# Optimization experiments

Hardware: AMD Instinct MI355X
Metric: run time of the kernel (lower is better)

The kernel has to match this reference:

```python
import jax, jax.numpy as jnp
import numpy as np

N = 16384
IN_DIM = 32
HID = 32
OUT_DIM = 16
BN_EPS = 1e-5


def setup_inputs() -> dict:
    key = jax.random.key(0)
    ks = jax.random.split(key, 8)
    x = jax.random.normal(ks[0], (N, IN_DIM), dtype=jnp.float32)
    # binary adjacency (edge existence only); avg degree ~33
    adj = jax.random.bernoulli(ks[1], 0.002, (N, N)).astype(jnp.int32)
    W1 = jax.random.normal(ks[2], (IN_DIM, HID), dtype=jnp.float32) * 0.05
    b1 = jnp.zeros((HID,), dtype=jnp.float32)
    gamma = jnp.ones((HID,), dtype=jnp.float32)
    beta = jnp.zeros((HID,), dtype=jnp.float32)
    W2 = jax.random.normal(ks[3], (HID, HID), dtype=jnp.float32) * 0.05
    b2 = jnp.zeros((HID,), dtype=jnp.float32)
    Wf = jax.random.normal(ks[4], (HID, OUT_DIM), dtype=jnp.float32) * 0.05
    bf = jnp.zeros((OUT_DIM,), dtype=jnp.float32)
    return {"x": x, "adj": adj, "W1": W1, "b1": b1, "gamma": gamma,
            "beta": beta, "W2": W2, "b2": b2, "Wf": Wf, "bf": bf}


def reference(x, adj, W1, b1, gamma, beta, W2, b2, Wf, bf):
    # GIN aggregation: for edge (src=row, dst=col) in dense_to_sparse(adj),
    # agg[dst] = sum over src of x[src]  ==  adj^T @ x  (binary adj)
    a = adj.astype(x.dtype)
    agg = jnp.einsum('ji,jd->id', a, x)  # (N, IN_DIM)
    h = x + agg  # eps = 0 default in GINConv: (1+eps)*x + agg
    # MLP: Linear -> BatchNorm1d (training stats) -> ReLU -> Linear -> ReLU
    h = h @ W1 + b1  # (N, HID)
    mu = jnp.mean(h, axis=0)
    var = jnp.mean((h - mu) ** 2, axis=0)  # biased variance (torch training mode)
    h = (h - mu) * jax.lax.rsqrt(var + BN_EPS) * gamma + beta
    h = jax.nn.relu(h)
    h = jax.nn.relu(h @ W2 + b2)  # (N, HID)
    # global mean pool over the single graph, then FC
    h_pool = jnp.mean(h, axis=0, keepdims=True)  # (1, HID)
    return h_pool @ Wf + bf  # (1, OUT_DIM)
```

## Files before the change

### kernel.cpp

```cpp
#include <hip/hip_runtime.h>

#define NN 16384
#define DD 32
#define NJ 8
#define TPB1 128
#define JCH (NN / NJ)
#define TPB2 64

template<int ATOMIC>
__global__ __launch_bounds__(TPB1) void k_agg(const int* __restrict__ adj,
                                              const float* __restrict__ x,
                                              float* __restrict__ part) {
  const int i = blockIdx.x * TPB1 + threadIdx.x;
  const int c = blockIdx.y;
  const size_t j0 = (size_t)c * JCH;
  float acc[DD];
#pragma unroll
  for (int d = 0; d < DD; ++d) acc[d] = 0.f;
  int any = 0;
  const int* p = adj + j0 * NN + i;
  for (int jj = 0; jj < JCH; jj += 8) {
    int v[8];
#pragma unroll
    for (int u = 0; u < 8; ++u) v[u] = __builtin_nontemporal_load(p + (size_t)u * NN);
    p += (size_t)8 * NN;
#pragma unroll
    for (int u = 0; u < 8; ++u) {
      if (v[u]) {
        any = 1;
        const float4* xr = (const float4*)(x + (j0 + jj + u) * DD);
#pragma unroll
        for (int q = 0; q < 8; ++q) {
          float4 xv = xr[q];
          acc[4*q+0] += xv.x; acc[4*q+1] += xv.y;
          acc[4*q+2] += xv.z; acc[4*q+3] += xv.w;
        }
      }
    }
  }
  if (ATOMIC) {
    if (any) {
      float* dst = part + (size_t)i * DD;
#pragma unroll
      for (int d = 0; d < DD; ++d) atomicAdd(dst + d, acc[d]);
    }
  } else {
    float4* dst = (float4*)(part + ((size_t)c * NN + i) * DD);
#pragma unroll
    for (int q = 0; q < 8; ++q)
      dst[q] = make_float4(acc[4*q], acc[4*q+1], acc[4*q+2], acc[4*q+3]);
  }
}

__global__ __launch_bounds__(TPB2) void k_mlp1(const float* __restrict__ x,
                                               const float* __restrict__ part, int nbuf,
                                               const float* __restrict__ W1,
                                               const float* __restrict__ b1,
                                               float* __restrict__ h1,
                                               float* __restrict__ stats) {
  __shared__ float sW[DD * DD];
  __shared__ float sb[DD];
  for (int t = threadIdx.x; t < DD * DD; t += TPB2) sW[t] = W1[t];
  if (threadIdx.x < DD) sb[threadIdx.x] = b1[threadIdx.x];
  __syncthreads();
  const int i = blockIdx.x * TPB2 + threadIdx.x;
  float hin[DD];
  const float4* xr = (const float4*)(x + (size_t)i * DD);
#pragma unroll
  for (int q = 0; q < 8; ++q) {
    float4 v = xr[q];
    hin[4*q] = v.x; hin[4*q+1] = v.y; hin[4*q+2] = v.z; hin[4*q+3] = v.w;
  }
  for (int c = 0; c < nbuf; ++c) {
    const float4* pr = (const float4*)(part + ((size_t)c * NN + i) * DD);
#pragma unroll
    for (int q = 0; q < 8; ++q) {
      float4 v = pr[q];
      hin[4*q] += v.x; hin[4*q+1] += v.y; hin[4*q+2] += v.z; hin[4*q+3] += v.w;
    }
  }
  float h[DD];
#pragma unroll
  for (int d = 0; d < DD; ++d) h[d] = sb[d];
  const float4* sW4 = (const float4*)sW;
#pragma unroll 4
  for (int k = 0; k < DD; ++k) {
    float hk = hin[k];
#pragma unroll
    for (int q = 0; q < 8; ++q) {
      float4 w = sW4[k*8 + q];
      h[4*q+0] += hk*w.x; h[4*q+1] += hk*w.y;
      h[4*q+2] += hk*w.z; h[4*q+3] += hk*w.w;
    }
  }
  float4* hw = (float4*)(h1 + (size_t)i * DD);
#pragma unroll
  for (int q = 0; q < 8; ++q)
    hw[q] = make_float4(h[4*q], h[4*q+1], h[4*q+2], h[4*q+3]);
#pragma unroll
  for (int d = 0; d < DD; ++d) {
    float s = h[d], ss = h[d] * h[d];
#pragma unroll
    for (int off = 32; off > 0; off >>= 1) {
      s += __shfl_xor(s, off);
      ss += __shfl_xor(ss, off);
    }
    if (threadIdx.x == 0) {
      atomicAdd(&stats[d], s);
      atomicAdd(&stats[DD + d], ss);
    }
  }
}

__global__ void k_bn(const float* __restrict__ gamma, const float* __restrict__ beta,
                     float* __restrict__ stats) {
  int d = threadIdx.x;
  if (d < DD) {
    float mu = stats[d] * (1.0f / NN);
    float var = stats[DD + d] * (1.0f / NN) - mu * mu;
    float sc = gamma[d] * rsqrtf(var + 1e-5f);
    stats[96 + d] = sc;
    stats[128 + d] = beta[d] - mu * sc;
  }
}

__global__ __launch_bounds__(TPB2) void k_mlp2(const float* __restrict__ h1,
                                               const float* __restrict__ W2,
                                               const float* __restrict__ b2,
                                               float* __restrict__ stats) {
  __shared__ float sW[DD * DD];
  __shared__ float sb[DD], ssc[DD], ssh[DD];
  for (int t = threadIdx.x; t < DD * DD; t += TPB2) sW[t] = W2[t];
  if (threadIdx.x < DD) {
    sb[threadIdx.x] = b2[threadIdx.x];
    ssc[threadIdx.x] = stats[96 + threadIdx.x];
    ssh[threadIdx.x] = stats[128 + threadIdx.x];
  }
  __syncthreads();
  const int i = blockIdx.x * TPB2 + threadIdx.x;
  float hn[DD];
  const float4* hr = (const float4*)(h1 + (size_t)i * DD);
#pragma unroll
  for (int q = 0; q < 8; ++q) {
    float4 v = hr[q];
    hn[4*q] = v.x; hn[4*q+1] = v.y; hn[4*q+2] = v.z; hn[4*q+3] = v.w;
  }
#pragma unroll
  for (int d = 0; d < DD; ++d) hn[d] = fmaxf(hn[d] * ssc[d] + ssh[d], 0.f);
  float h[DD];
#pragma unroll
  for (int d = 0; d < DD; ++d) h[d] = sb[d];
  const float4* sW4 = (const float4*)sW;
#pragma unroll 4
  for (int k = 0; k < DD; ++k) {
    float hk = hn[k];
#pragma unroll
    for (int q = 0; q < 8; ++q) {
      float4 w = sW4[k*8 + q];
      h[4*q+0] += hk*w.x; h[4*q+1] += hk*w.y;
      h[4*q+2] += hk*w.z; h[4*q+3] += hk*w.w;
    }
  }
#pragma unroll
  for (int d = 0; d < DD; ++d) {
    float s = fmaxf(h[d], 0.f);
#pragma unroll
    for (int off = 32; off > 0; off >>= 1) s += __shfl_xor(s, off);
    if (threadIdx.x == 0) atomicAdd(&stats[64 + d], s);
  }
}

__global__ void k_fc(const float* __restrict__ stats, const float* __restrict__ Wf,
                     const float* __restrict__ bf, float* __restrict__ out) {
  int o = threadIdx.x;
  if (o < 16) {
    float acc = bf[o];
#pragma unroll
    for (int d = 0; d < DD; ++d)
      acc += stats[64 + d] * (1.0f / NN) * Wf[d * 16 + o];
    out[o] = acc;
  }
}

extern "C" void kernel_launch(void* const* d_in, const int* in_sizes, int n_in,
                              void* d_out, int out_size, void* d_ws, size_t ws_size,
                              hipStream_t stream) {
  const float* x     = (const float*)d_in[0];
  const int*   adj   = (const int*)d_in[1];
  const float* W1    = (const float*)d_in[2];
  const float* b1    = (const float*)d_in[3];
  const float* gamma = (const float*)d_in[4];
  const float* beta  = (const float*)d_in[5];
  const float* W2    = (const float*)d_in[6];
  const float* b2    = (const float*)d_in[7];
  const float* Wf    = (const float*)d_in[8];
  const float* bf    = (const float*)d_in[9];
  float* out = (float*)d_out;

  float* stats = (float*)d_ws;
  float* h1 = stats + 256;
  float* part = h1 + (size_t)NN * DD;
  const size_t base_bytes = (256 + (size_t)NN * DD) * sizeof(float);
  const size_t part_bytes = (size_t)NJ * NN * DD * sizeof(float);
  const bool use_partials = ws_size >= base_bytes + part_bytes;
  const int nbuf = use_partials ? NJ : 1;

  hipMemsetAsync(d_ws, 0, 256 * sizeof(float), stream);
  dim3 g1(NN / TPB1, NJ);
  if (use_partials) {
    k_agg<0><<<g1, TPB1, 0, stream>>>(adj, x, part);
  } else {
    hipMemsetAsync(part, 0, (size_t)NN * DD * sizeof(float), stream);
    k_agg<1><<<g1, TPB1, 0, stream>>>(adj, x, part);
  }
  k_mlp1<<<NN / TPB2, TPB2, 0, stream>>>(x, part, nbuf, W1, b1, h1, stats);
  k_bn<<<1, 64, 0, stream>>>(gamma, beta, stats);
  k_mlp2<<<NN / TPB2, TPB2, 0, stream>>>(h1, W2, b2, stats);
  k_fc<<<1, 64, 0, stream>>>(stats, Wf, bf, out);
}
```

Before: 1.639 ms.

## Stream adjacency with 16-byte loads and scatter neighbor features via atomics

The aggregation kernel now reads the dense adjacency with 128-bit vector loads, four columns per thread, over a 2D grid of column groups and 256-row chunks. For every nonzero entry it adds the source row's features straight into the destination's aggregate with per-element float atomics, replacing register accumulators and the 8 partial buffers. The workspace aggregate is zeroed up front, and mlp1 reads a single buffer. This raises per-load efficiency on the 1 GiB adjacency stream and parallelism, at the cost of roughly 17M atomic adds to contended addresses and nondeterministic summation order.

```diff
diff --git a/kernel.cpp b/kernel.cpp
--- a/kernel.cpp
+++ b/kernel.cpp
@@ -2,58 +2,50 @@
 
 #define NN 16384
 #define DD 32
-#define NJ 8
-#define TPB1 128
-#define JCH (NN / NJ)
+#define TPB1 256
+#define ROWS_PER_BLK 256
+#define UNROLL 8
 #define TPB2 64
 
-template<int ATOMIC>
+typedef int ivec4 __attribute__((ext_vector_type(4)));
+
 __global__ __launch_bounds__(TPB1) void k_agg(const int* __restrict__ adj,
                                               const float* __restrict__ x,
-                                              float* __restrict__ part) {
-  const int i = blockIdx.x * TPB1 + threadIdx.x;
-  const int c = blockIdx.y;
-  const size_t j0 = (size_t)c * JCH;
-  float acc[DD];
+                                              float* __restrict__ agg) {
+  const int tcol = blockIdx.x * TPB1 + threadIdx.x;
+  const int j0 = blockIdx.y * ROWS_PER_BLK;
+  const ivec4* base = (const ivec4*)adj;
+  for (int jj = 0; jj < ROWS_PER_BLK; jj += UNROLL) {
+    ivec4 v[UNROLL];
 #pragma unroll
-  for (int d = 0; d < DD; ++d) acc[d] = 0.f;
-  int any = 0;
-  const int* p = adj + j0 * NN + i;
-  for (int jj = 0; jj < JCH; jj += 8) {
-    int v[8];
+    for (int u = 0; u < UNROLL; ++u)
+      v[u] = __builtin_nontemporal_load(base + (size_t)(j0 + jj + u) * (NN / 4) + tcol);
 #pragma unroll
-    for (int u = 0; u < 8; ++u) v[u] = __builtin_nontemporal_load(p + (size_t)u * NN);
-    p += (size_t)8 * NN;
+    for (int u = 0; u < UNROLL; ++u) {
+      if (v[u].x | v[u].y | v[u].z | v[u].w) {
+        const float4* xr = (const float4*)(x + (size_t)(j0 + jj + u) * DD);
+        int comp[4] = {v[u].x, v[u].y, v[u].z, v[u].w};
 #pragma unroll
-    for (int u = 0; u < 8; ++u) {
-      if (v[u]) {
-        any = 1;
-        const float4* xr = (const float4*)(x + (j0 + jj + u) * DD);
+        for (int k = 0; k < 4; ++k) {
+          if (comp[k]) {
+            float* dst = agg + (size_t)(tcol * 4 + k) * DD;
 #pragma unroll
-        for (int q = 0; q < 8; ++q) {
-          float4 xv = xr[q];
-          acc[4*q+0] += xv.x; acc[4*q+1] += xv.y;
-          acc[4*q+2] += xv.z; acc[4*q+3] += xv.w;
+            for (int q = 0; q < 8; ++q) {
+              float4 xv = xr[q];
+              atomicAdd(dst + 4 * q + 0, xv.x);
+              atomicAdd(dst + 4 * q + 1, xv.y);
+              atomicAdd(dst + 4 * q + 2, xv.z);
+              atomicAdd(dst + 4 * q + 3, xv.w);
+            }
+          }
         }
       }
     }
   }
-  if (ATOMIC) {
-    if (any) {
-      float* dst = part + (size_t)i * DD;
-#pragma unroll
-      for (int d = 0; d < DD; ++d) atomicAdd(dst + d, acc[d]);
-    }
-  } else {
-    float4* dst = (float4*)(part + ((size_t)c * NN + i) * DD);
-#pragma unroll
-    for (int q = 0; q < 8; ++q)
-      dst[q] = make_float4(acc[4*q], acc[4*q+1], acc[4*q+2], acc[4*q+3]);
-  }
 }
 
 __global__ __launch_bounds__(TPB2) void k_mlp1(const float* __restrict__ x,
-                                               const float* __restrict__ part, int nbuf,
+                                               const float* __restrict__ agg,
                                                const float* __restrict__ W1,
                                                const float* __restrict__ b1,
                                                float* __restrict__ h1,
@@ -66,18 +58,12 @@
   const int i = blockIdx.x * TPB2 + threadIdx.x;
   float hin[DD];
   const float4* xr = (const float4*)(x + (size_t)i * DD);
+  const float4* ar = (const float4*)(agg + (size_t)i * DD);
 #pragma unroll
   for (int q = 0; q < 8; ++q) {
-    float4 v = xr[q];
-    hin[4*q] = v.x; hin[4*q+1] = v.y; hin[4*q+2] = v.z; hin[4*q+3] = v.w;
-  }
-  for (int c = 0; c < nbuf; ++c) {
-    const float4* pr = (const float4*)(part + ((size_t)c * NN + i) * DD);
-#pragma unroll
-    for (int q = 0; q < 8; ++q) {
-      float4 v = pr[q];
-      hin[4*q] += v.x; hin[4*q+1] += v.y; hin[4*q+2] += v.z; hin[4*q+3] += v.w;
-    }
+    float4 v = xr[q], a = ar[q];
+    hin[4*q]   = v.x + a.x; hin[4*q+1] = v.y + a.y;
+    hin[4*q+2] = v.z + a.z; hin[4*q+3] = v.w + a.w;
   }
   float h[DD];
 #pragma unroll
@@ -198,22 +184,14 @@
   float* out = (float*)d_out;
 
   float* stats = (float*)d_ws;
-  float* h1 = stats + 256;
-  float* part = h1 + (size_t)NN * DD;
-  const size_t base_bytes = (256 + (size_t)NN * DD) * sizeof(float);
-  const size_t part_bytes = (size_t)NJ * NN * DD * sizeof(float);
-  const bool use_partials = ws_size >= base_bytes + part_bytes;
-  const int nbuf = use_partials ? NJ : 1;
+  float* agg = stats + 256;
+  float* h1 = agg + (size_t)NN * DD;
 
-  hipMemsetAsync(d_ws, 0, 256 * sizeof(float), stream);
-  dim3 g1(NN / TPB1, NJ);
-  if (use_partials) {
-    k_agg<0><<<g1, TPB1, 0, stream>>>(adj, x, part);
-  } else {
-    hipMemsetAsync(part, 0, (size_t)NN * DD * sizeof(float), stream);
-    k_agg<1><<<g1, TPB1, 0, stream>>>(adj, x, part);
-  }
-  k_mlp1<<<NN / TPB2, TPB2, 0, stream>>>(x, part, nbuf, W1, b1, h1, stats);
+  (void)hipMemsetAsync(d_ws, 0, (256 + (size_t)NN * DD) * sizeof(float), stream);
+
+  dim3 g1(NN / (TPB1 * 4), NN / ROWS_PER_BLK);
+  k_agg<<<g1, TPB1, 0, stream>>>(adj, x, agg);
+  k_mlp1<<<NN / TPB2, TPB2, 0, stream>>>(x, agg, W1, b1, h1, stats);
   k_bn<<<1, 64, 0, stream>>>(gamma, beta, stats);
   k_mlp2<<<NN / TPB2, TPB2, 0, stream>>>(h1, W2, b2, stats);
   k_fc<<<1, 64, 0, stream>>>(stats, Wf, bf, out);
```

Measured after the change: 2.389 ms. 45.7% more time.
